# Kernel optimization log

Hardware: AMD Instinct MI355X
Metric: run time of the kernel (lower is better)

The kernel has to match this reference:

```python
import jax, jax.numpy as jnp
import numpy as np

TANH_CONST = 1.5  # tanh_constant in __init__
EPS = 1e-9


def setup_inputs() -> dict:
    key = jax.random.key(0)
    ks = jax.random.split(key, 6)
    B, H, NOPS, T = 8192, 100, 5, 512
    return {
        "x0": jax.random.uniform(ks[0], (B, H), dtype=jnp.float32),          # g_emb-style uniform start input
        "W_x": jax.random.normal(ks[1], (H, 4 * H), dtype=jnp.float32) * 0.1,  # LSTMCell kernel (no bias)
        "W_h": jax.random.normal(ks[2], (H, 4 * H), dtype=jnp.float32) * 0.1,  # LSTMCell recurrent kernel
        "W_ops": jax.random.normal(ks[3], (H, NOPS), dtype=jnp.float32) * 0.1, # dense_ops (no bias)
        "emb": jax.random.normal(ks[4], (NOPS + 1, H), dtype=jnp.float32),     # Embedding(num_ops+1, lstm_size)
        "u": jax.random.uniform(ks[5], (T, B, NOPS), dtype=jnp.float32),       # uniform noise -> Gumbel-max sampling
    }


def reference(x0, W_x, W_h, W_ops, emb, u):
    # Gumbel noise for categorical sampling (equiv. in distribution to tf.random.categorical)
    g = -jnp.log(-jnp.log(u + EPS) + EPS)  # [T, B, num_ops]
    B, H = x0.shape

    def step(carry, g_t):
        h, c, x = carry
        # Keras LSTMCell, use_bias=False: gate order (i, f, c, o)
        z = x @ W_x + h @ W_h                      # [B, 4H]
        zi, zf, zc, zo = jnp.split(z, 4, axis=-1)
        c_new = jax.nn.sigmoid(zf) * c + jax.nn.sigmoid(zi) * jnp.tanh(zc)
        h_new = jax.nn.sigmoid(zo) * jnp.tanh(c_new)
        logits = TANH_CONST * jnp.tanh(h_new @ W_ops)  # tanh_constant * tanh(dense_ops(h))
        op = jnp.argmax(logits + g_t, axis=-1)         # [B] sampled op ids
        logp = jax.nn.log_softmax(logits, axis=-1)
        cur = -jnp.take_along_axis(logp, op[:, None], axis=-1)[:, 0]  # sparse xent vs sampled label
        ent = jax.lax.stop_gradient(cur * jnp.exp(-cur))
        x_new = emb[op]                                # next-step input = embedding(op_id)
        return (h_new, c_new, x_new), (cur, ent, op)

    h0 = jnp.zeros((B, H), x0.dtype)
    c0 = jnp.zeros((B, H), x0.dtype)
    _, (curs, ents, ops) = jax.lax.scan(step, (h0, c0, x0), g)
    log_prob = curs.sum(0)   # [B] accumulated self.log_prob
    entropy = ents.sum(0)    # [B] accumulated self.entropy
    return log_prob, entropy, ops
```

## Files before the change

### kernel.cpp

```cpp
#include <hip/hip_runtime.h>
#include <cstdint>
#include <cstddef>

typedef __attribute__((ext_vector_type(8))) short short8;
typedef __attribute__((ext_vector_type(4))) short bfx4;
typedef __attribute__((ext_vector_type(4))) float f32x4;

#define HH     100
#define G4     400
#define NCOL   416
#define NTIL   26
#define KTN    3
#define KRES   96
#define BTOT   8192
#define TST    512
#define ROWS   32
#define NBLK   256
#define BLOCK  512
#define ZW     420
#define TANHC  1.5f
#define EPSF   1e-9f

__device__ unsigned short d_Bhi[NTIL*KTN*64*8];
__device__ unsigned short d_Blo[NTIL*KTN*64*8];
__device__ float d_Ep2[6*G4];
__device__ float d_WresG[NCOL*4];
__device__ float d_Z0[(size_t)BTOT*G4];

static __device__ __forceinline__ unsigned short bf16hi(float f){
  unsigned u = __float_as_uint(f);
  return (unsigned short)((u + 0x7FFFu + ((u>>16)&1u)) >> 16);
}
static __device__ __forceinline__ float bf16f(unsigned short s){
  return __uint_as_float(((unsigned)s)<<16);
}
static __device__ __forceinline__ float frcp(float x){ return __builtin_amdgcn_rcpf(x); }
static __device__ __forceinline__ float sigf(float x){ return frcp(1.0f + __expf(-x)); }
static __device__ __forceinline__ float tanh_f(float x){ return 1.0f - 2.0f*frcp(__expf(2.0f*x) + 1.0f); }


__global__ void setup_bpack(const float* __restrict__ Wh, const float* __restrict__ Wops){
  int idx = blockIdx.x*blockDim.x + threadIdx.x;
  if (idx >= NTIL*KTN*64) return;
  int tile = idx/(KTN*64), rem = idx - tile*(KTN*64), kt = rem>>6, ln = rem&63;
  int n = tile*16 + (ln & 15);
  #pragma unroll
  for (int i = 0; i < 8; ++i){
    int k = kt*32 + (ln>>4)*8 + i;
    float w = 0.f;
    if (n < G4)          w = Wh[k*G4 + n];
    else if (n < G4+5)   w = Wops[k*5 + (n - G4)];
    unsigned short hi = bf16hi(w);
    unsigned short lo = bf16hi(w - bf16f(hi));
    d_Bhi[idx*8+i] = hi;
    d_Blo[idx*8+i] = lo;
  }
}

__global__ void setup_misc(const float* __restrict__ emb, const float* __restrict__ Wx,
                           const float* __restrict__ Wh, const float* __restrict__ Wops){
  int idx = blockIdx.x*blockDim.x + threadIdx.x;
  if (idx < 6*G4){
    int e = idx/G4, r2 = idx - e*G4, je = r2>>2, g = r2&3;
    float s = 0.f;
    for (int k = 0; k < HH; ++k) s = fmaf(emb[e*HH+k], Wx[k*G4 + g*HH + je], s);
    d_Ep2[idx] = s;
  } else if (idx < 6*G4 + NCOL*4){
    int i = idx - 6*G4, n = i>>2, q = i&3;
    float w = 0.f;
    if (n < G4)        w = Wh[(KRES+q)*G4 + n];
    else if (n < G4+5) w = Wops[(KRES+q)*5 + (n - G4)];
    d_WresG[i] = w;
  }
}

__global__ __launch_bounds__(256) void setup_z0(const float* __restrict__ x0,
                                                const float* __restrict__ Wx){
  __shared__ float xs[64*101];
  const int bb = blockIdx.x * 64;
  for (int i = threadIdx.x; i < 64*HH; i += 256){
    int r = i/HH, k = i - r*HH;
    xs[r*101 + k] = x0[(size_t)(bb + r)*HH + k];
  }
  __syncthreads();
  const int bl = threadIdx.x & 63;
  for (int ng = threadIdx.x >> 6; ng < HH; ng += 4){
    f32x4 a = {0.f,0.f,0.f,0.f};
    for (int k = 0; k < HH; ++k){
      f32x4 w = *(const f32x4*)&Wx[k*G4 + ng*4];
      a += w * xs[bl*101 + k];
    }
    *(f32x4*)&d_Z0[(size_t)(bb + bl)*G4 + ng*4] = a;
  }
}


__global__ __launch_bounds__(BLOCK, 2) void rnn_main(
    const float* __restrict__ u, float* __restrict__ out)
{
  __shared__ __align__(16) float z_lds[ROWS*ZW];
  __shared__ __align__(16) unsigned short fhi[2*KTN*64*8];
  __shared__ __align__(16) unsigned short flo[2*KTN*64*8];
  __shared__ __align__(16) float h_res[4*ROWS];
  __shared__ __align__(16) float Ep2_l[6*G4];
  __shared__ __align__(16) float Wres_l[NCOL*4];
  __shared__ __align__(16) float gn_lds[ROWS*5];
  __shared__ int op_lds[ROWS];

  const int tid  = threadIdx.x;
  const int wave = tid >> 6;
  const int lane = tid & 63;
  const int cn   = lane & 15;
  const int q4   = lane >> 4;
  const int row0 = blockIdx.x * ROWS;
  const int rE   = tid & 31;

  for (int i = tid; i < 6*G4;   i += BLOCK) Ep2_l[i]  = d_Ep2[i];
  for (int i = tid; i < NCOL*4; i += BLOCK) Wres_l[i] = d_WresG[i];

  const int tb  = (wave==0) ? 23 : (wave < 6) ? 3*(wave-1) : 15 + 4*(wave-6);
  const int ntl = (wave >= 6) ? 4 : 3;
  const int ngt = (wave == 0) ? 2 : ntl;
  short8 bh[4][KTN], bl[4][KTN];
  {
    const short8* bph = (const short8*)d_Bhi;
    const short8* bpl = (const short8*)d_Blo;
    #pragma unroll
    for (int tl = 0; tl < 4; ++tl) if (tl < ntl)
      #pragma unroll
      for (int kt = 0; kt < KTN; ++kt){
        int fi = ((tb+tl)*KTN + kt)*64 + lane;
        bh[tl][kt] = bph[fi];
        bl[tl][kt] = bpl[fi];
      }
  }

  float cs1[4] = {0.f,0.f,0.f,0.f};
  float cs2[4] = {0.f,0.f,0.f,0.f};
  float lp_acc = 0.f, ent_acc = 0.f;

  for (int t = 0; t <= TST; ++t){
    float upr[5];
    if (t < TST && tid >= 416 && tid < 448){
      const float* up = u + ((size_t)t*BTOT + row0 + (tid - 416))*5;
      #pragma unroll
      for (int o = 0; o < 5; ++o) upr[o] = up[o];
    }

    if (t == 0){
      for (int i = tid; i < ROWS*HH; i += BLOCK){
        int r = i/HH, c4 = i - r*HH;
        *(f32x4*)&z_lds[r*ZW + c4*4] =
          *(const f32x4*)&d_Z0[(size_t)(row0 + r)*G4 + c4*4];
      }
    } else {
      f32x4 accT[2];
      #pragma unroll
      for (int mt = 0; mt < 2; ++mt){
        short8 ah[KTN], al[KTN];
        #pragma unroll
        for (int kt = 0; kt < KTN; ++kt){
          ah[kt] = *(const short8*)&fhi[((mt*KTN + kt)*64 + lane)*8];
          al[kt] = *(const short8*)&flo[((mt*KTN + kt)*64 + lane)*8];
        }
        f32x4 hq[4];
        #pragma unroll
        for (int q = 0; q < 4; ++q)
          hq[q] = *(const f32x4*)&h_res[q*ROWS + mt*16 + q4*4];
        #pragma unroll
        for (int tl = 0; tl < 4; ++tl) if (tl < ngt){
          const int n = (tb+tl)*16 + cn;
          f32x4 acc = {0.f,0.f,0.f,0.f};
          #pragma unroll
          for (int kt = 0; kt < KTN; ++kt){
            acc = __builtin_amdgcn_mfma_f32_16x16x32_bf16(ah[kt], bh[tl][kt], acc, 0,0,0);
            acc = __builtin_amdgcn_mfma_f32_16x16x32_bf16(al[kt], bh[tl][kt], acc, 0,0,0);
            acc = __builtin_amdgcn_mfma_f32_16x16x32_bf16(ah[kt], bl[tl][kt], acc, 0,0,0);
          }
          f32x4 wr = *(const f32x4*)&Wres_l[n*4];
          #pragma unroll
          for (int q = 0; q < 4; ++q) acc += hq[q] * wr[q];
          const int rowb = mt*16 + q4*4;
          #pragma unroll
          for (int i = 0; i < 4; ++i)
            z_lds[(rowb + i)*ZW + n] = acc[i];
        }
        if (wave == 0){
          f32x4 a = {0.f,0.f,0.f,0.f};
          #pragma unroll
          for (int kt = 0; kt < KTN; ++kt){
            a = __builtin_amdgcn_mfma_f32_16x16x32_bf16(bh[2][kt], ah[kt], a, 0,0,0);
            a = __builtin_amdgcn_mfma_f32_16x16x32_bf16(bh[2][kt], al[kt], a, 0,0,0);
            a = __builtin_amdgcn_mfma_f32_16x16x32_bf16(bl[2][kt], ah[kt], a, 0,0,0);
          }
          accT[mt] = a;
        }
      }
      if (wave == 0){
        #pragma unroll
        for (int mt = 0; mt < 2; ++mt){
          const int rr = mt*16 + cn;
          float h0 = h_res[0*ROWS + rr], h1 = h_res[1*ROWS + rr];
          float h2 = h_res[2*ROWS + rr], h3 = h_res[3*ROWS + rr];
          #pragma unroll
          for (int i = 0; i < 4; ++i){
            f32x4 wr = *(const f32x4*)&Wres_l[(G4 + q4*4 + i)*4];
            accT[mt][i] += h0*wr.x + h1*wr.y + h2*wr.z + h3*wr.w;
          }
        }
        float o4lo = __shfl_down(accT[0][0], 16);
        float t1o0 = __shfl_up(accT[1][0], 16);
        float t1o1 = __shfl_up(accT[1][1], 16);
        float t1o2 = __shfl_up(accT[1][2], 16);
        float t1o3 = __shfl_up(accT[1][3], 16);
        if (lane < 32){
          const int r = lane;
          float raw[5];
          if (lane < 16){
            raw[0] = accT[0][0]; raw[1] = accT[0][1];
            raw[2] = accT[0][2]; raw[3] = accT[0][3]; raw[4] = o4lo;
          } else {
            raw[0] = t1o0; raw[1] = t1o1; raw[2] = t1o2; raw[3] = t1o3;
            raw[4] = accT[1][0];
          }
          float l[5];
          #pragma unroll
          for (int o = 0; o < 5; ++o) l[o] = TANHC * tanh_f(raw[o]);
          int op = 0; float best = -1e30f;
          #pragma unroll
          for (int o = 0; o < 5; ++o){
            float v = l[o] + gn_lds[r*5 + o];
            if (v > best){ best = v; op = o; }
          }
          float mx = fmaxf(fmaxf(fmaxf(l[0],l[1]), fmaxf(l[2],l[3])), l[4]);
          float se = 0.f;
          #pragma unroll
          for (int o = 0; o < 5; ++o) se += __expf(l[o] - mx);
          float lse = mx + __logf(se);
          float cur = lse - l[op];
          lp_acc  += cur;
          ent_acc += cur * __expf(-cur);
          op_lds[r] = op;
          out[2*BTOT + (size_t)(t-1)*BTOT + row0 + r] = (float)op;
        }
      }
    }
    if (t == TST) break;
    __syncthreads();

    const int opv = (t > 0) ? op_lds[rE] : 0;
    {
      const int jg = tid >> 5;
      f32x4 zg[4];
      #pragma unroll
      for (int g = 0; g < 4; ++g)
        zg[g] = *(const f32x4*)&z_lds[rE*ZW + g*HH + jg*4];
      if (t > 0){
        #pragma unroll
        for (int i = 0; i < 4; ++i){
          f32x4 e4 = *(const f32x4*)&Ep2_l[opv*G4 + (jg*4 + i)*4];
          zg[0][i] += e4.x; zg[1][i] += e4.y; zg[2][i] += e4.z; zg[3][i] += e4.w;
        }
      }
      float hv[4];
      #pragma unroll
      for (int i = 0; i < 4; ++i){
        float cn_ = sigf(zg[1][i])*cs1[i] + sigf(zg[0][i])*tanh_f(zg[2][i]);
        cs1[i] = cn_;
        hv[i] = sigf(zg[3][i])*tanh_f(cn_);
      }
      bfx4 h4, l4;
      #pragma unroll
      for (int i = 0; i < 4; ++i){
        unsigned short hi = bf16hi(hv[i]);
        h4[i] = (short)hi;
        l4[i] = (short)bf16hi(hv[i] - bf16f(hi));
      }
      const int kt   = jg >> 3;
      const int lf   = (rE & 15) | (((jg >> 1) & 3) << 4);
      const int mt   = rE >> 4;
      const int j0   = (jg & 1) * 4;
      const int base = ((mt*KTN + kt)*64 + lf)*8 + j0;
      *(bfx4*)&fhi[base] = h4;
      *(bfx4*)&flo[base] = l4;
    }
    if (tid < 256 || tid >= 480){
      const int jg = (tid < 256) ? (16 + (tid >> 5)) : 24;
      const int c0 = jg*4;
      f32x4 zg[4];
      #pragma unroll
      for (int g = 0; g < 4; ++g)
        zg[g] = *(const f32x4*)&z_lds[rE*ZW + g*HH + c0];
      if (t > 0){
        #pragma unroll
        for (int i = 0; i < 4; ++i){
          f32x4 e4 = *(const f32x4*)&Ep2_l[opv*G4 + (c0 + i)*4];
          zg[0][i] += e4.x; zg[1][i] += e4.y; zg[2][i] += e4.z; zg[3][i] += e4.w;
        }
      }
      float hv[4];
      #pragma unroll
      for (int i = 0; i < 4; ++i){
        float cn_ = sigf(zg[1][i])*cs2[i] + sigf(zg[0][i])*tanh_f(zg[2][i]);
        cs2[i] = cn_;
        hv[i] = sigf(zg[3][i])*tanh_f(cn_);
      }
      if (tid < 256){
        bfx4 h4, l4;
        #pragma unroll
        for (int i = 0; i < 4; ++i){
          unsigned short hi = bf16hi(hv[i]);
          h4[i] = (short)hi;
          l4[i] = (short)bf16hi(hv[i] - bf16f(hi));
        }
        const int kt   = jg >> 3;
        const int lf   = (rE & 15) | (((jg >> 1) & 3) << 4);
        const int mt   = rE >> 4;
        const int j0   = (jg & 1) * 4;
        const int base = ((mt*KTN + kt)*64 + lf)*8 + j0;
        *(bfx4*)&fhi[base] = h4;
        *(bfx4*)&flo[base] = l4;
      } else {
        #pragma unroll
        for (int i = 0; i < 4; ++i) h_res[i*ROWS + rE] = hv[i];
      }
    } else if (tid >= 416 && tid < 448){
      int r = tid - 416;
      #pragma unroll
      for (int o = 0; o < 5; ++o)
        gn_lds[r*5 + o] = -__logf(-__logf(upr[o] + EPSF) + EPSF);
    }
    __syncthreads();
  }

  if (wave == 0 && lane < 32){
    out[row0 + lane]        = lp_acc;
    out[BTOT + row0 + lane] = ent_acc;
  }
}

extern "C" void kernel_launch(void* const* d_in, const int* in_sizes, int n_in,
                              void* d_out, int out_size, void* d_ws, size_t ws_size,
                              hipStream_t stream) {
  const float* x0   = (const float*)d_in[0];
  const float* Wx   = (const float*)d_in[1];
  const float* Wh   = (const float*)d_in[2];
  const float* Wops = (const float*)d_in[3];
  const float* emb  = (const float*)d_in[4];
  const float* u    = (const float*)d_in[5];
  (void)d_ws; (void)ws_size; (void)in_sizes; (void)n_in;

  setup_bpack<<<(NTIL*KTN*64 + 255)/256, 256, 0, stream>>>(Wh, Wops);
  setup_misc<<<(6*G4 + NCOL*4 + 255)/256, 256, 0, stream>>>(emb, Wx, Wh, Wops);
  setup_z0<<<BTOT/64, 256, 0, stream>>>(x0, Wx);
  rnn_main<<<NBLK, BLOCK, 0, stream>>>(u, (float*)d_out);
}
```

Baseline: 1.986 ms.

## Pad K to 128 in MFMA tiles, drop fp32 residual, prioritize logits in wave 0

Extends the recurrent matmul K dimension from 96 to 128 with zero-padded weights and zero-initialized h fragments, so the last four hidden units go through MFMA instead of a separate fp32 residual path. This removes the h_res/Wres LDS buffers and per-tile residual FMAs, and wave 0 now computes the logits tile and sampling before its gate tiles to shorten the critical path. It costs a third more MFMA instructions per tile.

Result: faster. 1.873 ms (-5.7%).

```diff
diff --git a/kernel.cpp b/kernel.cpp
--- a/kernel.cpp
+++ b/kernel.cpp
@@ -8,23 +8,21 @@
 
 #define HH     100
 #define G4     400
-#define NCOL   416
 #define NTIL   26
-#define KTN    3
-#define KRES   96
+#define KTN    4
 #define BTOT   8192
 #define TST    512
 #define ROWS   32
 #define NBLK   256
 #define BLOCK  512
 #define ZW     420
+#define EPW    404
 #define TANHC  1.5f
 #define EPSF   1e-9f
 
 __device__ unsigned short d_Bhi[NTIL*KTN*64*8];
 __device__ unsigned short d_Blo[NTIL*KTN*64*8];
-__device__ float d_Ep2[6*G4];
-__device__ float d_WresG[NCOL*4];
+__device__ float d_Ep2[6*EPW];
 __device__ float d_Z0[(size_t)BTOT*G4];
 
 static __device__ __forceinline__ unsigned short bf16hi(float f){
@@ -48,8 +46,10 @@
   for (int i = 0; i < 8; ++i){
     int k = kt*32 + (ln>>4)*8 + i;
     float w = 0.f;
-    if (n < G4)          w = Wh[k*G4 + n];
-    else if (n < G4+5)   w = Wops[k*5 + (n - G4)];
+    if (k < HH){
+      if (n < G4)          w = Wh[k*G4 + n];
+      else if (n < G4+5)   w = Wops[k*5 + (n - G4)];
+    }
     unsigned short hi = bf16hi(w);
     unsigned short lo = bf16hi(w - bf16f(hi));
     d_Bhi[idx*8+i] = hi;
@@ -57,20 +57,14 @@
   }
 }
 
-__global__ void setup_misc(const float* __restrict__ emb, const float* __restrict__ Wx,
-                           const float* __restrict__ Wh, const float* __restrict__ Wops){
+__global__ void setup_misc(const float* __restrict__ emb, const float* __restrict__ Wx){
   int idx = blockIdx.x*blockDim.x + threadIdx.x;
-  if (idx < 6*G4){
-    int e = idx/G4, r2 = idx - e*G4, je = r2>>2, g = r2&3;
+  if (idx < 6*EPW){
+    int e = idx/EPW, r2 = idx - e*EPW, je = r2>>2, g = r2&3;
     float s = 0.f;
-    for (int k = 0; k < HH; ++k) s = fmaf(emb[e*HH+k], Wx[k*G4 + g*HH + je], s);
+    if (je < HH)
+      for (int k = 0; k < HH; ++k) s = fmaf(emb[e*HH+k], Wx[k*G4 + g*HH + je], s);
     d_Ep2[idx] = s;
-  } else if (idx < 6*G4 + NCOL*4){
-    int i = idx - 6*G4, n = i>>2, q = i&3;
-    float w = 0.f;
-    if (n < G4)        w = Wh[(KRES+q)*G4 + n];
-    else if (n < G4+5) w = Wops[(KRES+q)*5 + (n - G4)];
-    d_WresG[i] = w;
   }
 }
 
@@ -101,9 +95,7 @@
   __shared__ __align__(16) float z_lds[ROWS*ZW];
   __shared__ __align__(16) unsigned short fhi[2*KTN*64*8];
   __shared__ __align__(16) unsigned short flo[2*KTN*64*8];
-  __shared__ __align__(16) float h_res[4*ROWS];
-  __shared__ __align__(16) float Ep2_l[6*G4];
-  __shared__ __align__(16) float Wres_l[NCOL*4];
+  __shared__ __align__(16) float Ep2_l[6*EPW];
   __shared__ __align__(16) float gn_lds[ROWS*5];
   __shared__ int op_lds[ROWS];
 
@@ -115,12 +107,12 @@
   const int row0 = blockIdx.x * ROWS;
   const int rE   = tid & 31;
 
-  for (int i = tid; i < 6*G4;   i += BLOCK) Ep2_l[i]  = d_Ep2[i];
-  for (int i = tid; i < NCOL*4; i += BLOCK) Wres_l[i] = d_WresG[i];
+  for (int i = tid; i < 6*EPW; i += BLOCK) Ep2_l[i] = d_Ep2[i];
+  for (int i = tid; i < 2*KTN*64*8; i += BLOCK){ fhi[i] = 0; flo[i] = 0; }
 
   const int tb  = (wave==0) ? 23 : (wave < 6) ? 3*(wave-1) : 15 + 4*(wave-6);
-  const int ntl = (wave >= 6) ? 4 : 3;
-  const int ngt = (wave == 0) ? 2 : ntl;
+  const int ntl = (wave==0) ? 3 : (wave < 6) ? 3 : 4;
+  const int ngt = (wave==0) ? 2 : ntl;
   short8 bh[4][KTN], bl[4][KTN];
   {
     const short8* bph = (const short8*)d_Bhi;
@@ -153,7 +145,7 @@
         *(f32x4*)&z_lds[r*ZW + c4*4] =
           *(const f32x4*)&d_Z0[(size_t)(row0 + r)*G4 + c4*4];
       }
-    } else {
+    } else if (wave == 0){
       f32x4 accT[2];
       #pragma unroll
       for (int mt = 0; mt < 2; ++mt){
@@ -163,10 +155,83 @@
           ah[kt] = *(const short8*)&fhi[((mt*KTN + kt)*64 + lane)*8];
           al[kt] = *(const short8*)&flo[((mt*KTN + kt)*64 + lane)*8];
         }
-        f32x4 hq[4];
-        #pragma unroll
-        for (int q = 0; q < 4; ++q)
-          hq[q] = *(const f32x4*)&h_res[q*ROWS + mt*16 + q4*4];
+        f32x4 a = {0.f,0.f,0.f,0.f};
+        #pragma unroll
+        for (int kt = 0; kt < KTN; ++kt){
+          a = __builtin_amdgcn_mfma_f32_16x16x32_bf16(bh[2][kt], ah[kt], a, 0,0,0);
+          a = __builtin_amdgcn_mfma_f32_16x16x32_bf16(bh[2][kt], al[kt], a, 0,0,0);
+          a = __builtin_amdgcn_mfma_f32_16x16x32_bf16(bl[2][kt], ah[kt], a, 0,0,0);
+        }
+        accT[mt] = a;
+      }
+      float o4lo = __shfl_down(accT[0][0], 16);
+      float t1o0 = __shfl_up(accT[1][0], 16);
+      float t1o1 = __shfl_up(accT[1][1], 16);
+      float t1o2 = __shfl_up(accT[1][2], 16);
+      float t1o3 = __shfl_up(accT[1][3], 16);
+      if (lane < 32){
+        const int r = lane;
+        float raw[5];
+        if (lane < 16){
+          raw[0] = accT[0][0]; raw[1] = accT[0][1];
+          raw[2] = accT[0][2]; raw[3] = accT[0][3]; raw[4] = o4lo;
+        } else {
+          raw[0] = t1o0; raw[1] = t1o1; raw[2] = t1o2; raw[3] = t1o3;
+          raw[4] = accT[1][0];
+        }
+        float l[5];
+        #pragma unroll
+        for (int o = 0; o < 5; ++o) l[o] = TANHC * tanh_f(raw[o]);
+        int op = 0; float best = -1e30f;
+        #pragma unroll
+        for (int o = 0; o < 5; ++o){
+          float v = l[o] + gn_lds[r*5 + o];
+          if (v > best){ best = v; op = o; }
+        }
+        float mx = fmaxf(fmaxf(fmaxf(l[0],l[1]), fmaxf(l[2],l[3])), l[4]);
+        float se = 0.f;
+        #pragma unroll
+        for (int o = 0; o < 5; ++o) se += __expf(l[o] - mx);
+        float lse = mx + __logf(se);
+        float cur = lse - l[op];
+        lp_acc  += cur;
+        ent_acc += cur * __expf(-cur);
+        op_lds[r] = op;
+        out[2*BTOT + (size_t)(t-1)*BTOT + row0 + r] = (float)op;
+      }
+      #pragma unroll
+      for (int mt = 0; mt < 2; ++mt){
+        short8 ah[KTN], al[KTN];
+        #pragma unroll
+        for (int kt = 0; kt < KTN; ++kt){
+          ah[kt] = *(const short8*)&fhi[((mt*KTN + kt)*64 + lane)*8];
+          al[kt] = *(const short8*)&flo[((mt*KTN + kt)*64 + lane)*8];
+        }
+        #pragma unroll
+        for (int tl = 0; tl < 2; ++tl){
+          const int n = (23+tl)*16 + cn;
+          f32x4 acc = {0.f,0.f,0.f,0.f};
+          #pragma unroll
+          for (int kt = 0; kt < KTN; ++kt){
+            acc = __builtin_amdgcn_mfma_f32_16x16x32_bf16(ah[kt], bh[tl][kt], acc, 0,0,0);
+            acc = __builtin_amdgcn_mfma_f32_16x16x32_bf16(al[kt], bh[tl][kt], acc, 0,0,0);
+            acc = __builtin_amdgcn_mfma_f32_16x16x32_bf16(ah[kt], bl[tl][kt], acc, 0,0,0);
+          }
+          const int rowb = mt*16 + q4*4;
+          #pragma unroll
+          for (int i = 0; i < 4; ++i)
+            z_lds[(rowb + i)*ZW + n] = acc[i];
+        }
+      }
+    } else {
+      #pragma unroll
+      for (int mt = 0; mt < 2; ++mt){
+        short8 ah[KTN], al[KTN];
+        #pragma unroll
+        for (int kt = 0; kt < KTN; ++kt){
+          ah[kt] = *(const short8*)&fhi[((mt*KTN + kt)*64 + lane)*8];
+          al[kt] = *(const short8*)&flo[((mt*KTN + kt)*64 + lane)*8];
+        }
         #pragma unroll
         for (int tl = 0; tl < 4; ++tl) if (tl < ngt){
           const int n = (tb+tl)*16 + cn;
@@ -177,72 +242,11 @@
             acc = __builtin_amdgcn_mfma_f32_16x16x32_bf16(al[kt], bh[tl][kt], acc, 0,0,0);
             acc = __builtin_amdgcn_mfma_f32_16x16x32_bf16(ah[kt], bl[tl][kt], acc, 0,0,0);
           }
-          f32x4 wr = *(const f32x4*)&Wres_l[n*4];
-          #pragma unroll
-          for (int q = 0; q < 4; ++q) acc += hq[q] * wr[q];
           const int rowb = mt*16 + q4*4;
           #pragma unroll
           for (int i = 0; i < 4; ++i)
             z_lds[(rowb + i)*ZW + n] = acc[i];
         }
-        if (wave == 0){
-          f32x4 a = {0.f,0.f,0.f,0.f};
-          #pragma unroll
-          for (int kt = 0; kt < KTN; ++kt){
-            a = __builtin_amdgcn_mfma_f32_16x16x32_bf16(bh[2][kt], ah[kt], a, 0,0,0);
-            a = __builtin_amdgcn_mfma_f32_16x16x32_bf16(bh[2][kt], al[kt], a, 0,0,0);
-            a = __builtin_amdgcn_mfma_f32_16x16x32_bf16(bl[2][kt], ah[kt], a, 0,0,0);
-          }
-          accT[mt] = a;
-        }
-      }
-      if (wave == 0){
-        #pragma unroll
-        for (int mt = 0; mt < 2; ++mt){
-          const int rr = mt*16 + cn;
-          float h0 = h_res[0*ROWS + rr], h1 = h_res[1*ROWS + rr];
-          float h2 = h_res[2*ROWS + rr], h3 = h_res[3*ROWS + rr];
-          #pragma unroll
-          for (int i = 0; i < 4; ++i){
-            f32x4 wr = *(const f32x4*)&Wres_l[(G4 + q4*4 + i)*4];
-            accT[mt][i] += h0*wr.x + h1*wr.y + h2*wr.z + h3*wr.w;
-          }
-        }
-        float o4lo = __shfl_down(accT[0][0], 16);
-        float t1o0 = __shfl_up(accT[1][0], 16);
-        float t1o1 = __shfl_up(accT[1][1], 16);
-        float t1o2 = __shfl_up(accT[1][2], 16);
-        float t1o3 = __shfl_up(accT[1][3], 16);
-        if (lane < 32){
-          const int r = lane;
-          float raw[5];
-          if (lane < 16){
-            raw[0] = accT[0][0]; raw[1] = accT[0][1];
-            raw[2] = accT[0][2]; raw[3] = accT[0][3]; raw[4] = o4lo;
-          } else {
-            raw[0] = t1o0; raw[1] = t1o1; raw[2] = t1o2; raw[3] = t1o3;
-            raw[4] = accT[1][0];
-          }
-          float l[5];
-          #pragma unroll
-          for (int o = 0; o < 5; ++o) l[o] = TANHC * tanh_f(raw[o]);
-          int op = 0; float best = -1e30f;
-          #pragma unroll
-          for (int o = 0; o < 5; ++o){
-            float v = l[o] + gn_lds[r*5 + o];
-            if (v > best){ best = v; op = o; }
-          }
-          float mx = fmaxf(fmaxf(fmaxf(l[0],l[1]), fmaxf(l[2],l[3])), l[4]);
-          float se = 0.f;
-          #pragma unroll
-          for (int o = 0; o < 5; ++o) se += __expf(l[o] - mx);
-          float lse = mx + __logf(se);
-          float cur = lse - l[op];
-          lp_acc  += cur;
-          ent_acc += cur * __expf(-cur);
-          op_lds[r] = op;
-          out[2*BTOT + (size_t)(t-1)*BTOT + row0 + r] = (float)op;
-        }
       }
     }
     if (t == TST) break;
@@ -258,7 +262,7 @@
       if (t > 0){
         #pragma unroll
         for (int i = 0; i < 4; ++i){
-          f32x4 e4 = *(const f32x4*)&Ep2_l[opv*G4 + (jg*4 + i)*4];
+          f32x4 e4 = *(const f32x4*)&Ep2_l[opv*EPW + (jg*4 + i)*4];
           zg[0][i] += e4.x; zg[1][i] += e4.y; zg[2][i] += e4.z; zg[3][i] += e4.w;
         }
       }
@@ -284,17 +288,16 @@
       *(bfx4*)&fhi[base] = h4;
       *(bfx4*)&flo[base] = l4;
     }
-    if (tid < 256 || tid >= 480){
-      const int jg = (tid < 256) ? (16 + (tid >> 5)) : 24;
-      const int c0 = jg*4;
+    if (tid < 288){
+      const int jg = 16 + (tid >> 5);
       f32x4 zg[4];
       #pragma unroll
       for (int g = 0; g < 4; ++g)
-        zg[g] = *(const f32x4*)&z_lds[rE*ZW + g*HH + c0];
+        zg[g] = *(const f32x4*)&z_lds[rE*ZW + g*HH + jg*4];
       if (t > 0){
         #pragma unroll
         for (int i = 0; i < 4; ++i){
-          f32x4 e4 = *(const f32x4*)&Ep2_l[opv*G4 + (c0 + i)*4];
+          f32x4 e4 = *(const f32x4*)&Ep2_l[opv*EPW + (jg*4 + i)*4];
           zg[0][i] += e4.x; zg[1][i] += e4.y; zg[2][i] += e4.z; zg[3][i] += e4.w;
         }
       }
@@ -305,25 +308,20 @@
         cs2[i] = cn_;
         hv[i] = sigf(zg[3][i])*tanh_f(cn_);
       }
-      if (tid < 256){
-        bfx4 h4, l4;
-        #pragma unroll
-        for (int i = 0; i < 4; ++i){
-          unsigned short hi = bf16hi(hv[i]);
-          h4[i] = (short)hi;
-          l4[i] = (short)bf16hi(hv[i] - bf16f(hi));
-        }
-        const int kt   = jg >> 3;
-        const int lf   = (rE & 15) | (((jg >> 1) & 3) << 4);
-        const int mt   = rE >> 4;
-        const int j0   = (jg & 1) * 4;
-        const int base = ((mt*KTN + kt)*64 + lf)*8 + j0;
-        *(bfx4*)&fhi[base] = h4;
-        *(bfx4*)&flo[base] = l4;
-      } else {
-        #pragma unroll
-        for (int i = 0; i < 4; ++i) h_res[i*ROWS + rE] = hv[i];
-      }
+      bfx4 h4, l4;
+      #pragma unroll
+      for (int i = 0; i < 4; ++i){
+        unsigned short hi = bf16hi(hv[i]);
+        h4[i] = (short)hi;
+        l4[i] = (short)bf16hi(hv[i] - bf16f(hi));
+      }
+      const int kt   = jg >> 3;
+      const int lf   = (rE & 15) | (((jg >> 1) & 3) << 4);
+      const int mt   = rE >> 4;
+      const int j0   = (jg & 1) * 4;
+      const int base = ((mt*KTN + kt)*64 + lf)*8 + j0;
+      *(bfx4*)&fhi[base] = h4;
+      *(bfx4*)&flo[base] = l4;
     } else if (tid >= 416 && tid < 448){
       int r = tid - 416;
       #pragma unroll
@@ -351,7 +349,7 @@
   (void)d_ws; (void)ws_size; (void)in_sizes; (void)n_in;
 
   setup_bpack<<<(NTIL*KTN*64 + 255)/256, 256, 0, stream>>>(Wh, Wops);
-  setup_misc<<<(6*G4 + NCOL*4 + 255)/256, 256, 0, stream>>>(emb, Wx, Wh, Wops);
+  setup_misc<<<(6*EPW + 255)/256, 256, 0, stream>>>(emb, Wx);
   setup_z0<<<BTOT/64, 256, 0, stream>>>(x0, Wx);
   rnn_main<<<NBLK, BLOCK, 0, stream>>>(u, (float*)d_out);
 }
```
